# Optimization experiments

Hardware: AMD Instinct MI355X
Metric: run time of the kernel (lower is better)

The kernel has to match this reference:

```python
import jax, jax.numpy as jnp
import numpy as np

N_NODES = 50000
N_EDGES = 600000
DIM = 128
N_LAYERS = 5


def setup_inputs() -> dict:
    key = jax.random.key(0)
    k1, k2, k3, k4 = jax.random.split(key, 4)
    x = jax.random.normal(k1, (N_NODES, DIM), dtype=jnp.float32)
    edge_index = jax.random.randint(k2, (2, N_EDGES), 0, N_NODES, dtype=jnp.int64)
    # small init scale to keep 5-layer activations numerically sane
    W_l = jax.random.normal(k3, (N_LAYERS, DIM, DIM), dtype=jnp.float32) * 0.05
    W_r = jax.random.normal(k4, (N_LAYERS, DIM, DIM), dtype=jnp.float32) * 0.05
    b_l = jnp.zeros((N_LAYERS, DIM), dtype=jnp.float32)
    return {"x": x, "edge_index": edge_index, "W_l": W_l, "b_l": b_l, "W_r": W_r}


def reference(x, edge_index, W_l, b_l, W_r):
    """GraphSAGE forward: 5 stacked SAGEConv (mean aggr) + relu between layers.
    Dropout is identity (eval mode). SAGEConv: out = lin_l(mean_j x_j) + lin_r(x_i).
    """
    src = edge_index[0]  # message sources (x_j)
    dst = edge_index[1]  # aggregation targets (x_i)
    n = x.shape[0]
    # in-degree for mean aggregation (clamped to avoid div-by-zero)
    deg = jax.ops.segment_sum(jnp.ones_like(dst, dtype=x.dtype), dst, num_segments=n)
    inv_deg = 1.0 / jnp.maximum(deg, 1.0)  # [N]
    n_layers = W_l.shape[0]
    for i in range(n_layers):
        msg = x[src]  # [E, D] gather
        aggr = jax.ops.segment_sum(msg, dst, num_segments=n) * inv_deg[:, None]  # [N, D]
        x = aggr @ W_l[i] + b_l[i] + x @ W_r[i]
        if i < n_layers - 1:
            x = jax.nn.relu(x)
    return x
```

## Files before the change

kernel.cpp:

```cpp
#include <hip/hip_runtime.h>

#define NDIM 128

typedef __attribute__((ext_vector_type(8))) short s16x8;
typedef __attribute__((ext_vector_type(8))) _Float16 h16x8;
typedef __attribute__((ext_vector_type(4))) float f32x4;

__device__ __forceinline__ unsigned short f2h(float f) {
    _Float16 h = (_Float16)f;
    return *(unsigned short*)&h;
}
__device__ __forceinline__ float h2f(unsigned short u) {
    _Float16 h = *(_Float16*)&u;
    return (float)h;
}

__device__ __forceinline__ void g2lds16(const void* g, void* l) {
    __builtin_amdgcn_global_load_lds(
        (const __attribute__((address_space(1))) void*)g,
        (__attribute__((address_space(3))) void*)l, 16, 0, 0);
}

__global__ __launch_bounds__(256) void init_detect_kernel(
    const int* __restrict__ raw, int* __restrict__ deg, int* __restrict__ flag,
    int E, int N) {
    const int tid = threadIdx.x;
    const int gtid = blockIdx.x * 256 + tid;
    const int gsz = gridDim.x * 256;
    for (int i = gtid; i < N; i += gsz) deg[i] = 0;
    if (blockIdx.x == 0) {
        __shared__ int any_nz;
        if (tid == 0) any_nz = 0;
        __syncthreads();
        int local = 0;
        const int samples = (E < 4096) ? E : 4096;
#pragma unroll
        for (int j = 0; j < 16; ++j) {
            int i = tid * 16 + j;
            if (i < samples) local |= raw[2 * i + 1];
        }
        if (local) atomicOr(&any_nz, 1);
        __syncthreads();
        if (tid == 0) *flag = any_nz;
    }
}

__global__ void convert_kernel(const int* __restrict__ raw, const int* __restrict__ flag,
                               int* __restrict__ idx, int* __restrict__ deg, int E) {
    int i = blockIdx.x * 256 + threadIdx.x;
    if (i >= 2 * E) return;
    int v = (*flag == 0) ? raw[2 * i] : raw[i];
    idx[i] = v;
    if (i >= E) atomicAdd(&deg[v], 1);
}

__global__ __launch_bounds__(256) void deg_reduce_kernel(
    const int* __restrict__ deg, int* __restrict__ partials, int n) {
    const int base = blockIdx.x * 1024;
    const int tid = threadIdx.x;
    int s = 0;
#pragma unroll
    for (int j = 0; j < 4; ++j) {
        int i = base + tid * 4 + j;
        if (i < n) s += deg[i];
    }
#pragma unroll
    for (int off = 32; off; off >>= 1) s += __shfl_down(s, off);
    __shared__ int ws[4];
    if ((tid & 63) == 0) ws[tid >> 6] = s;
    __syncthreads();
    if (tid == 0) partials[blockIdx.x] = ws[0] + ws[1] + ws[2] + ws[3];
}

__global__ void scan_partials_kernel(int* __restrict__ partials, int nb,
                                     int* __restrict__ row_start, int n) {
    __shared__ int sh[1024];
    const int tid = threadIdx.x;
    int v = (tid < nb) ? partials[tid] : 0;
    sh[tid] = v;
    __syncthreads();
    for (int off = 1; off < 1024; off <<= 1) {
        int a = sh[tid];
        int b = (tid >= off) ? sh[tid - off] : 0;
        __syncthreads();
        sh[tid] = a + b;
        __syncthreads();
    }
    if (tid < nb) partials[tid] = (tid == 0) ? 0 : sh[tid - 1];
    if (tid == 0) row_start[n] = sh[1023];
}

__global__ __launch_bounds__(256) void deg_downsweep_kernel(
    const int* __restrict__ deg, const int* __restrict__ partials,
    int* __restrict__ row_start, int* __restrict__ cursor,
    float* __restrict__ inv_deg, int n) {
    const int base = blockIdx.x * 1024;
    const int tid = threadIdx.x;
    const int i0 = base + tid * 4;
    int d[4];
    int s = 0;
#pragma unroll
    for (int j = 0; j < 4; ++j) {
        int i = i0 + j;
        d[j] = (i < n) ? deg[i] : 0;
        s += d[j];
    }
    const int lane = tid & 63;
    int incl = s;
#pragma unroll
    for (int off = 1; off < 64; off <<= 1) {
        int t = __shfl_up(incl, off);
        if (lane >= off) incl += t;
    }
    __shared__ int wsum[4];
    if (lane == 63) wsum[tid >> 6] = incl;
    __syncthreads();
    int woff = 0;
    const int w = tid >> 6;
    for (int k = 0; k < w; ++k) woff += wsum[k];
    int excl = incl - s + woff + partials[blockIdx.x];
#pragma unroll
    for (int j = 0; j < 4; ++j) {
        int i = i0 + j;
        if (i < n) {
            row_start[i] = excl;
            cursor[i] = excl;
            inv_deg[i] = 1.0f / (float)max(d[j], 1);
            excl += d[j];
        }
    }
}

__global__ __launch_bounds__(256) void scatter_kernel(
    const int* __restrict__ idx, int* __restrict__ cursor,
    int* __restrict__ sorted_src, int E) {
    const int i0 = (blockIdx.x * 256 + threadIdx.x) * 8;
    if (i0 >= E) return;
    int s[8], d[8], p[8];
#pragma unroll
    for (int j = 0; j < 8; ++j) {
        if (i0 + j < E) {
            s[j] = idx[i0 + j];
            d[j] = idx[E + i0 + j];
        }
    }
#pragma unroll
    for (int j = 0; j < 8; ++j)
        if (i0 + j < E) p[j] = atomicAdd(&cursor[d[j]], 1);
#pragma unroll
    for (int j = 0; j < 8; ++j)
        if (i0 + j < E) sorted_src[p[j]] = s[j];
}

__global__ __launch_bounds__(256) void prep_kernel(
    const float* __restrict__ Wl, const float* __restrict__ Wr,
    short* __restrict__ wfrag,
    const float* __restrict__ X, short* __restrict__ Xf16, int total4) {
    int t = blockIdx.x * 256 + threadIdx.x;
    if (t < 327680) {
        int j = t & 7;
        int lane = (t >> 3) & 63;
        int ct = (t >> 9) & 7;
        int chunk = (t >> 12) & 3;
        int plane = (t >> 14) & 3;
        int l = t >> 16;
        int nn = ct * 16 + (lane & 15);
        int k = chunk * 32 + (lane >> 4) * 8 + j;
        const float* src = (plane < 2) ? Wl : Wr;
        float v = src[(size_t)l * 16384 + (size_t)k * 128 + nn];
        unsigned short h = f2h(v);
        wfrag[t] = (plane & 1) ? (short)f2h((v - h2f(h)) * 2048.0f) : (short)h;
    } else {
        int i = t - 327680;
        if (i >= total4) return;
        float4 v = *(const float4*)(X + (size_t)i * 4);
        unsigned short f[4] = {f2h(v.x), f2h(v.y), f2h(v.z), f2h(v.w)};
        *(int2*)(Xf16 + (size_t)i * 4) = make_int2(
            (int)(f[0] | ((unsigned)f[1] << 16)), (int)(f[2] | ((unsigned)f[3] << 16)));
    }
}

__global__ __launch_bounds__(256) void aggregate_kernel(
    const short* __restrict__ Xf16, const int* __restrict__ row_start,
    const int* __restrict__ sorted_src, const float* __restrict__ inv_deg,
    short* __restrict__ Agf16, int n) {
    int gid = blockIdx.x * 256 + threadIdx.x;
    int node = gid >> 5;
    if (node >= n) return;
    const int lane32 = threadIdx.x & 31;
    const int q = lane32 << 2;
    const int beg = row_start[node];
    const int end = row_start[node + 1];
    float4 acc = make_float4(0.f, 0.f, 0.f, 0.f);
    for (int base = beg; base < end; base += 32) {
        const int cnt = min(end - base, 32);
        const int my_src = (lane32 < cnt) ? sorted_src[base + lane32] : 0;
        for (int jb = 0; jb < cnt; jb += 8) {
            int2 v[8];
            float m[8];
#pragma unroll
            for (int t = 0; t < 8; ++t) {
                const int j = jb + t;
                const int js = (j < cnt) ? j : (cnt - 1);
                const int s = __shfl(my_src, js, 32);
                v[t] = *(const int2*)(Xf16 + (size_t)s * 128 + q);
                m[t] = (j < cnt) ? 1.f : 0.f;
            }
#pragma unroll
            for (int t = 0; t < 8; ++t) {
                union { int2 i2; _Float16 h[4]; } u;
                u.i2 = v[t];
                acc.x = fmaf(m[t], (float)u.h[0], acc.x);
                acc.y = fmaf(m[t], (float)u.h[1], acc.y);
                acc.z = fmaf(m[t], (float)u.h[2], acc.z);
                acc.w = fmaf(m[t], (float)u.h[3], acc.w);
            }
        }
    }
    const float inv = inv_deg[node];
    acc.x *= inv; acc.y *= inv; acc.z *= inv; acc.w *= inv;
    unsigned short f[4] = {f2h(acc.x), f2h(acc.y), f2h(acc.z), f2h(acc.w)};
    *(int2*)(Agf16 + (size_t)node * 128 + q) = make_int2(
        (int)(f[0] | ((unsigned)f[1] << 16)), (int)(f[2] | ((unsigned)f[3] << 16)));
}

__global__ __launch_bounds__(256, 4) void gemm_kernel(
    const short* __restrict__ Agf16, const short* __restrict__ Xf16,
    const short* __restrict__ wfrag,
    const float* __restrict__ bias,
    float* __restrict__ Yf, short* __restrict__ Yf16,
    int n, int do_relu) {
    __shared__ __align__(16) short sT[2][64][64];
    const int tid = threadIdx.x;
    const int lane = tid & 63;
    const int wave = tid >> 6;
    const int ln15 = lane & 15;
    const int quad = lane >> 4;
    const int row0 = blockIdx.x * 64;
    const int wr0 = (wave & 1) * 32;
    const int wc0 = (wave >> 1) * 64;
    const int ctbase = (wave >> 1) * 4;

    f32x4 accM[2][4], accR[2][4];
#pragma unroll
    for (int i = 0; i < 2; ++i)
#pragma unroll
        for (int j = 0; j < 4; ++j) { accM[i][j] = (f32x4)(0.f); accR[i][j] = (f32x4)(0.f); }

    const short* pbase = (wave < 2) ? Agf16 : Xf16;
    const int rhalf = (wave & 1) * 32;
    const int rl = lane >> 3;
    const int gslot = (lane & 7) ^ rl;

    for (int kp = 0; kp < 2; ++kp) {
        __syncthreads();
#pragma unroll
        for (int i = 0; i < 4; ++i) {
            const int rloc = rhalf + i * 8;
            int grow = row0 + rloc + rl;
            if (grow >= n) grow = n - 1;
            const short* g = pbase + (size_t)grow * 128 + kp * 64 + gslot * 8;
            g2lds16(g, &sT[wave >> 1][rloc][0]);
        }
        __syncthreads();

#pragma unroll
        for (int ch = 0; ch < 2; ++ch) {
            const int chunk = kp * 2 + ch;
            h16x8 fAg[2], fX[2];
#pragma unroll
            for (int rt = 0; rt < 2; ++rt) {
                const int r = wr0 + rt * 16 + ln15;
                const int cc = (ch * 4 + quad) ^ (r & 7);
                fAg[rt] = *(const h16x8*)&sT[0][r][cc * 8];
                fX[rt]  = *(const h16x8*)&sT[1][r][cc * 8];
            }
#pragma unroll
            for (int ct = 0; ct < 4; ++ct) {
                const short* wb = wfrag + (chunk << 12) + ((ctbase + ct) << 9) + (lane << 3);
                const h16x8 wlh = *(const h16x8*)(wb);
                const h16x8 wll = *(const h16x8*)(wb + 16384);
                const h16x8 wrh = *(const h16x8*)(wb + 32768);
                const h16x8 wrl = *(const h16x8*)(wb + 49152);
#pragma unroll
                for (int rt = 0; rt < 2; ++rt) {
                    accM[rt][ct] = __builtin_amdgcn_mfma_f32_16x16x32_f16(fAg[rt], wlh, accM[rt][ct], 0, 0, 0);
                    accR[rt][ct] = __builtin_amdgcn_mfma_f32_16x16x32_f16(fAg[rt], wll, accR[rt][ct], 0, 0, 0);
                    accM[rt][ct] = __builtin_amdgcn_mfma_f32_16x16x32_f16(fX[rt],  wrh, accM[rt][ct], 0, 0, 0);
                    accR[rt][ct] = __builtin_amdgcn_mfma_f32_16x16x32_f16(fX[rt],  wrl, accR[rt][ct], 0, 0, 0);
                }
            }
        }
    }

#pragma unroll
    for (int rt = 0; rt < 2; ++rt) {
#pragma unroll
        for (int ct = 0; ct < 4; ++ct) {
            const int col = wc0 + ct * 16 + ln15;
            const float bv = bias[col];
#pragma unroll
            for (int r = 0; r < 4; ++r) {
                const int grow = row0 + wr0 + rt * 16 + quad * 4 + r;
                if (grow < n) {
                    float v = accM[rt][ct][r] + accR[rt][ct][r] * 4.8828125e-4f + bv;
                    if (do_relu) v = fmaxf(v, 0.f);
                    if (Yf) {
                        Yf[(size_t)grow * NDIM + col] = v;
                    } else {
                        Yf16[(size_t)grow * 128 + col] = (short)f2h(v);
                    }
                }
            }
        }
    }
}

extern "C" void kernel_launch(void* const* d_in, const int* in_sizes, int n_in,
                              void* d_out, int out_size, void* d_ws, size_t ws_size,
                              hipStream_t stream) {
    const float* x0   = (const float*)d_in[0];
    const int*   eraw = (const int*)d_in[1];
    const float* Wl   = (const float*)d_in[2];
    const float* bl   = (const float*)d_in[3];
    const float* Wr   = (const float*)d_in[4];
    float* out = (float*)d_out;

    const int N = in_sizes[0] / NDIM;
    const int E = in_sizes[1] / 2;

    auto align_up = [](size_t v) { return (v + 255) & ~(size_t)255; };
    char* p = (char*)d_ws;
    int* idx = (int*)p;                 p += align_up((size_t)2 * E * 4);
    int* deg = (int*)p;                 p += align_up((size_t)(N + 1) * 4);
    int* flag = deg + N;
    int* row_start = (int*)p;           p += align_up((size_t)(N + 1) * 4);
    int* cursor = (int*)p;              p += align_up((size_t)N * 4);
    int* ssrc = (int*)p;                p += align_up((size_t)E * 4);
    float* invd = (float*)p;            p += align_up((size_t)N * 4);
    int* partials = (int*)p;            p += align_up((size_t)1024 * 4);
    short* wfrag = (short*)p;           p += align_up((size_t)327680 * 2);
    short* f16[3];
    for (int s = 0; s < 3; ++s) {
        f16[s] = (short*)p;             p += align_up((size_t)N * 128 * 2);
    }

    const int nb = (N + 1023) / 1024;
    const int preptotal = 327680 + N * 32;

    init_detect_kernel<<<256, 256, 0, stream>>>(eraw, deg, flag, E, N);
    convert_kernel<<<(2 * E + 255) / 256, 256, 0, stream>>>(eraw, flag, idx, deg, E);
    deg_reduce_kernel<<<nb, 256, 0, stream>>>(deg, partials, N);
    scan_partials_kernel<<<1, 1024, 0, stream>>>(partials, nb, row_start, N);
    deg_downsweep_kernel<<<nb, 256, 0, stream>>>(deg, partials, row_start, cursor, invd, N);
    scatter_kernel<<<(E + 2047) / 2048, 256, 0, stream>>>(idx, cursor, ssrc, E);
    prep_kernel<<<(preptotal + 255) / 256, 256, 0, stream>>>(
        Wl, Wr, wfrag, x0, f16[0], N * 32);

    int xs = 0;
    for (int l = 0; l < 5; ++l) {
        const int as_ = (xs + 1) % 3;
        const int ys = (xs + 2) % 3;
        aggregate_kernel<<<(N * 32 + 255) / 256, 256, 0, stream>>>(
            f16[xs], row_start, ssrc, invd, f16[as_], N);
        if (l < 4) {
            gemm_kernel<<<(N + 63) / 64, 256, 0, stream>>>(
                f16[as_], f16[xs], wfrag + (size_t)l * 65536,
                bl + (size_t)l * NDIM, nullptr, f16[ys], N, 1);
        } else {
            gemm_kernel<<<(N + 63) / 64, 256, 0, stream>>>(
                f16[as_], f16[xs], wfrag + (size_t)l * 65536,
                bl + (size_t)l * NDIM, out, nullptr, N, 0);
        }
        xs = ys;
    }
}
```

Measured before the change: 358.5 us.

## Widen aggregate loads to 16 bytes per lane and shrink GEMM row tile to 32

The aggregate kernel now gives each node 16 lanes, each loading 8 halves (16 bytes) per neighbor instead of 32 lanes loading 4 halves. This halves the thread count and shuffle work per gathered row and doubles the bytes in flight per lane. The GEMM kernel now uses 32-row tiles with each wave covering all rows and 32 columns. That doubles the grid and cuts per-block LDS and accumulator registers, at the cost of more weight-fragment reloads per output row.

Result: no change. 361.8 us (+0.9%).

```diff
diff --git a/kernel.cpp b/kernel.cpp
--- a/kernel.cpp
+++ b/kernel.cpp
@@ -185,43 +185,44 @@
     const int* __restrict__ sorted_src, const float* __restrict__ inv_deg,
     short* __restrict__ Agf16, int n) {
     int gid = blockIdx.x * 256 + threadIdx.x;
-    int node = gid >> 5;
+    int node = gid >> 4;
     if (node >= n) return;
-    const int lane32 = threadIdx.x & 31;
-    const int q = lane32 << 2;
+    const int lane16 = threadIdx.x & 15;
+    const int q = lane16 << 3;
     const int beg = row_start[node];
     const int end = row_start[node + 1];
-    float4 acc = make_float4(0.f, 0.f, 0.f, 0.f);
-    for (int base = beg; base < end; base += 32) {
-        const int cnt = min(end - base, 32);
-        const int my_src = (lane32 < cnt) ? sorted_src[base + lane32] : 0;
+    float acc[8] = {0.f, 0.f, 0.f, 0.f, 0.f, 0.f, 0.f, 0.f};
+    for (int base = beg; base < end; base += 16) {
+        const int cnt = min(end - base, 16);
+        const int my_src = (lane16 < cnt) ? sorted_src[base + lane16] : 0;
         for (int jb = 0; jb < cnt; jb += 8) {
-            int2 v[8];
+            int4 v[8];
             float m[8];
 #pragma unroll
             for (int t = 0; t < 8; ++t) {
                 const int j = jb + t;
                 const int js = (j < cnt) ? j : (cnt - 1);
-                const int s = __shfl(my_src, js, 32);
-                v[t] = *(const int2*)(Xf16 + (size_t)s * 128 + q);
+                const int s = __shfl(my_src, js, 16);
+                v[t] = *(const int4*)(Xf16 + (size_t)s * 128 + q);
                 m[t] = (j < cnt) ? 1.f : 0.f;
             }
 #pragma unroll
             for (int t = 0; t < 8; ++t) {
-                union { int2 i2; _Float16 h[4]; } u;
-                u.i2 = v[t];
-                acc.x = fmaf(m[t], (float)u.h[0], acc.x);
-                acc.y = fmaf(m[t], (float)u.h[1], acc.y);
-                acc.z = fmaf(m[t], (float)u.h[2], acc.z);
-                acc.w = fmaf(m[t], (float)u.h[3], acc.w);
+                union { int4 i4; _Float16 h[8]; } u;
+                u.i4 = v[t];
+#pragma unroll
+                for (int e = 0; e < 8; ++e)
+                    acc[e] = fmaf(m[t], (float)u.h[e], acc[e]);
             }
         }
     }
     const float inv = inv_deg[node];
-    acc.x *= inv; acc.y *= inv; acc.z *= inv; acc.w *= inv;
-    unsigned short f[4] = {f2h(acc.x), f2h(acc.y), f2h(acc.z), f2h(acc.w)};
-    *(int2*)(Agf16 + (size_t)node * 128 + q) = make_int2(
-        (int)(f[0] | ((unsigned)f[1] << 16)), (int)(f[2] | ((unsigned)f[3] << 16)));
+    unsigned short f[8];
+#pragma unroll
+    for (int e = 0; e < 8; ++e) f[e] = f2h(acc[e] * inv);
+    *(int4*)(Agf16 + (size_t)node * 128 + q) = make_int4(
+        (int)(f[0] | ((unsigned)f[1] << 16)), (int)(f[2] | ((unsigned)f[3] << 16)),
+        (int)(f[4] | ((unsigned)f[5] << 16)), (int)(f[6] | ((unsigned)f[7] << 16)));
 }
 
 __global__ __launch_bounds__(256, 4) void gemm_kernel(
@@ -230,32 +231,31 @@
     const float* __restrict__ bias,
     float* __restrict__ Yf, short* __restrict__ Yf16,
     int n, int do_relu) {
-    __shared__ __align__(16) short sT[2][64][64];
+    __shared__ __align__(16) short sT[2][32][64];
     const int tid = threadIdx.x;
     const int lane = tid & 63;
     const int wave = tid >> 6;
     const int ln15 = lane & 15;
     const int quad = lane >> 4;
-    const int row0 = blockIdx.x * 64;
-    const int wr0 = (wave & 1) * 32;
-    const int wc0 = (wave >> 1) * 64;
-    const int ctbase = (wave >> 1) * 4;
-
-    f32x4 accM[2][4], accR[2][4];
+    const int row0 = blockIdx.x * 32;
+    const int wc0 = wave * 32;
+    const int ctbase = wave * 2;
+
+    f32x4 accM[2][2], accR[2][2];
 #pragma unroll
     for (int i = 0; i < 2; ++i)
 #pragma unroll
-        for (int j = 0; j < 4; ++j) { accM[i][j] = (f32x4)(0.f); accR[i][j] = (f32x4)(0.f); }
+        for (int j = 0; j < 2; ++j) { accM[i][j] = (f32x4)(0.f); accR[i][j] = (f32x4)(0.f); }
 
     const short* pbase = (wave < 2) ? Agf16 : Xf16;
-    const int rhalf = (wave & 1) * 32;
+    const int rhalf = (wave & 1) * 16;
     const int rl = lane >> 3;
     const int gslot = (lane & 7) ^ rl;
 
     for (int kp = 0; kp < 2; ++kp) {
         __syncthreads();
 #pragma unroll
-        for (int i = 0; i < 4; ++i) {
+        for (int i = 0; i < 2; ++i) {
             const int rloc = rhalf + i * 8;
             int grow = row0 + rloc + rl;
             if (grow >= n) grow = n - 1;
@@ -270,13 +270,13 @@
             h16x8 fAg[2], fX[2];
 #pragma unroll
             for (int rt = 0; rt < 2; ++rt) {
-                const int r = wr0 + rt * 16 + ln15;
+                const int r = rt * 16 + ln15;
                 const int cc = (ch * 4 + quad) ^ (r & 7);
                 fAg[rt] = *(const h16x8*)&sT[0][r][cc * 8];
                 fX[rt]  = *(const h16x8*)&sT[1][r][cc * 8];
             }
 #pragma unroll
-            for (int ct = 0; ct < 4; ++ct) {
+            for (int ct = 0; ct < 2; ++ct) {
                 const short* wb = wfrag + (chunk << 12) + ((ctbase + ct) << 9) + (lane << 3);
                 const h16x8 wlh = *(const h16x8*)(wb);
                 const h16x8 wll = *(const h16x8*)(wb + 16384);
@@ -296,12 +296,12 @@
 #pragma unroll
     for (int rt = 0; rt < 2; ++rt) {
 #pragma unroll
-        for (int ct = 0; ct < 4; ++ct) {
+        for (int ct = 0; ct < 2; ++ct) {
             const int col = wc0 + ct * 16 + ln15;
             const float bv = bias[col];
 #pragma unroll
             for (int r = 0; r < 4; ++r) {
-                const int grow = row0 + wr0 + rt * 16 + quad * 4 + r;
+                const int grow = row0 + rt * 16 + quad * 4 + r;
                 if (grow < n) {
                     float v = accM[rt][ct][r] + accR[rt][ct][r] * 4.8828125e-4f + bv;
                     if (do_relu) v = fmaxf(v, 0.f);
@@ -361,14 +361,14 @@
     for (int l = 0; l < 5; ++l) {
         const int as_ = (xs + 1) % 3;
         const int ys = (xs + 2) % 3;
-        aggregate_kernel<<<(N * 32 + 255) / 256, 256, 0, stream>>>(
+        aggregate_kernel<<<(N * 16 + 255) / 256, 256, 0, stream>>>(
             f16[xs], row_start, ssrc, invd, f16[as_], N);
         if (l < 4) {
-            gemm_kernel<<<(N + 63) / 64, 256, 0, stream>>>(
+            gemm_kernel<<<(N + 31) / 32, 256, 0, stream>>>(
                 f16[as_], f16[xs], wfrag + (size_t)l * 65536,
                 bl + (size_t)l * NDIM, nullptr, f16[ys], N, 1);
         } else {
-            gemm_kernel<<<(N + 63) / 64, 256, 0, stream>>>(
+            gemm_kernel<<<(N + 31) / 32, 256, 0, stream>>>(
                 f16[as_], f16[xs], wfrag + (size_t)l * 65536,
                 bl + (size_t)l * NDIM, out, nullptr, N, 0);
         }
```
